# Optimization experiments

Measured on AMD Instinct MI355X. Metric: run time of the kernel, lower is better.

## Reference

```python
import jax, jax.numpy as jnp
import numpy as np

B, S, D_MODEL, HEADS = 2, 2048, 1024, 16
K_D = D_MODEL // HEADS


def setup_inputs() -> dict:
    key = jax.random.key(0)
    ks = jax.random.split(key, 5)
    x = jax.random.normal(ks[0], (B, S, D_MODEL), dtype=jnp.float32)
    # causal mask, 1 = keep, 0 = masked (GPT-2 style)
    mask = jnp.tril(jnp.ones((S, S), dtype=jnp.int32))[None, None, :, :]
    sc = 0.02
    w_attn = jax.random.normal(ks[1], (D_MODEL, 3 * D_MODEL), dtype=jnp.float32) * sc
    b_attn = jax.random.normal(ks[2], (3 * D_MODEL,), dtype=jnp.float32) * sc
    w_proj = jax.random.normal(ks[3], (D_MODEL, D_MODEL), dtype=jnp.float32) * sc
    b_proj = jax.random.normal(ks[4], (D_MODEL,), dtype=jnp.float32) * sc
    return {"x": x, "mask": mask, "w_attn": w_attn, "b_attn": b_attn,
            "w_proj": w_proj, "b_proj": b_proj}


def reference(x, mask, w_attn, b_attn, w_proj, b_proj):
    b, s, _ = x.shape
    qkv = x @ w_attn + b_attn                      # [B,S,3*d_model]
    # NOTE: source assigns value, query, key = split(...) in that order
    v, q, k = jnp.split(qkv, 3, axis=-1)
    def heads(t):  # [B,S,d_model] -> [B,H,S,k_d]
        return t.reshape(b, s, HEADS, K_D).transpose(0, 2, 1, 3)
    v, q, k = heads(v), heads(q), heads(k)
    present = jnp.stack((k, v))                    # [2,B,H,S,k_d]
    scores = jnp.einsum('bhqd,bhkd->bhqk', q, k) / jnp.sqrt(jnp.float32(K_D))
    scores = jnp.where(mask == 0, -jnp.inf, scores)
    attn = jax.nn.softmax(scores, axis=-1)         # [B,H,S,S]
    out = jnp.einsum('bhqk,bhkd->bhqd', attn, v)   # [B,H,S,k_d]
    out = out.transpose(0, 2, 1, 3).reshape(b, s, D_MODEL)
    out = out @ w_proj + b_proj
    return out, present
```

## Files before the change

### kernel.cpp

```cpp
#include <hip/hip_runtime.h>
#include <math.h>

constexpr int BB = 2;
constexpr int SS = 2048;
constexpr int DM = 1024;
constexpr int NH = 16;
constexpr int KD = 64;
constexpr int OUT_ELEMS  = BB*SS*DM;
constexpr int PRES_HALF  = BB*NH*SS*KD;
#define NEGSENT (-1e30f)

typedef __attribute__((ext_vector_type(8))) short short8;
typedef __attribute__((ext_vector_type(4))) short short4v;
typedef __attribute__((ext_vector_type(4))) float f32x4;

__device__ __forceinline__ float us2f(unsigned short u) {
  union { unsigned int ui; float f; } c; c.ui = ((unsigned int)u) << 16; return c.f;
}
__device__ __forceinline__ short f2s(float f) {
  union { float f; unsigned int u; } c; c.f = f;
  return (short)((c.u + 0x7FFFu + ((c.u >> 16) & 1u)) >> 16);
}

#define GLOAD_LDS16(g, l) \
  __builtin_amdgcn_global_load_lds((const __attribute__((address_space(1))) void*)(g), \
                                   (__attribute__((address_space(3))) void*)(l), 16, 0, 0)

__global__ __launch_bounds__(256)
void cast_x_k(const float* __restrict__ x, short* __restrict__ xb) {
  const size_t i = ((size_t)blockIdx.x * 256 + threadIdx.x) * 4;
  const float4 v = *(const float4*)(x + i);
  short4v s; s.x = f2s(v.x); s.y = f2s(v.y); s.z = f2s(v.z); s.w = f2s(v.w);
  *(short4v*)(xb + i) = s;
}

__global__ __launch_bounds__(256)
void transpose_k(const float* __restrict__ w, int N, short* __restrict__ wt) {
  __shared__ float tl[32][33];
  const int tx = threadIdx.x & 31, ty = threadIdx.x >> 5;
  const int n0 = blockIdx.x * 32, k0 = blockIdx.y * 32;
  #pragma unroll
  for (int i = 0; i < 4; ++i) {
    const int kk = ty + i * 8;
    tl[kk][tx] = w[(size_t)(k0 + kk) * N + n0 + tx];
  }
  __syncthreads();
  #pragma unroll
  for (int i = 0; i < 4; ++i) {
    const int nn = ty + i * 8;
    wt[(size_t)(n0 + nn) * 1024 + k0 + tx] = f2s(tl[tx][nn]);
  }
}

__device__ __forceinline__ void mfma_tile_loop(
    const short* __restrict__ A, const short* __restrict__ Bt,
    int m0, int n0, short* Asm, short* Bsm, f32x4 (*acc)[4]) {
  const int tid = threadIdx.x;
  const int lane = tid & 63;
  const int w = tid >> 6;
  const int wm = (w >> 1) * 64, wn = (w & 1) * 64;
  const int ln15 = lane & 15, quad = lane >> 4;
  for (int k0 = 0; k0 < 1024; k0 += 32) {
    #pragma unroll
    for (int j = 0; j < 2; ++j) {
      const int e = j * 256 + tid;
      const int r = e >> 2, cq = e & 3;
      GLOAD_LDS16(A  + (size_t)(m0 + r) * 1024 + k0 + cq * 8, Asm + e * 8);
      GLOAD_LDS16(Bt + (size_t)(n0 + r) * 1024 + k0 + cq * 8, Bsm + e * 8);
    }
    __syncthreads();
    short8 af[4], bf[4];
    #pragma unroll
    for (int t = 0; t < 4; ++t)
      af[t] = *(const short8*)(Asm + (wm + t * 16 + ln15) * 32 + quad * 8);
    #pragma unroll
    for (int t = 0; t < 4; ++t)
      bf[t] = *(const short8*)(Bsm + (wn + t * 16 + ln15) * 32 + quad * 8);
    #pragma unroll
    for (int tm = 0; tm < 4; ++tm)
      #pragma unroll
      for (int tn = 0; tn < 4; ++tn)
        acc[tm][tn] = __builtin_amdgcn_mfma_f32_16x16x32_bf16(
            af[tm], bf[tn], acc[tm][tn], 0, 0, 0);
    __syncthreads();
  }
}

__global__ __launch_bounds__(256)
void qkv_mfma_k(const short* __restrict__ A, const short* __restrict__ Bt,
                const float* __restrict__ bias, short* __restrict__ qbf,
                float* __restrict__ outf, short* __restrict__ kbf,
                short* __restrict__ vbft) {
  __shared__ short Asm[128 * 32];
  __shared__ short Bsm[128 * 32];
  const int n0 = blockIdx.x * 128, m0 = blockIdx.y * 128;
  f32x4 acc[4][4] = {};
  mfma_tile_loop(A, Bt, m0, n0, Asm, Bsm, acc);
  const int lane = threadIdx.x & 63;
  const int w = threadIdx.x >> 6;
  const int wm = (w >> 1) * 64, wn = (w & 1) * 64;
  const int col = lane & 15, row4 = (lane >> 4) * 4;
  #pragma unroll
  for (int tm = 0; tm < 4; ++tm) {
    #pragma unroll
    for (int tn = 0; tn < 4; ++tn) {
      const int n = n0 + wn + tn * 16 + col;
      #pragma unroll
      for (int r = 0; r < 4; ++r) {
        const int m = m0 + wm + tm * 16 + row4 + r;
        const float val = acc[tm][tn][r] + bias[n];
        const int bb = m >> 11, s = m & 2047;
        const int c = n & 1023, h = c >> 6, d = c & 63;
        const size_t idx = ((size_t)(bb * NH + h) * SS + s) * KD + d;
        if (n < DM) {
          outf[(size_t)OUT_ELEMS + (size_t)PRES_HALF + idx] = val;
          if (kbf) vbft[((size_t)(bb * NH + h) * KD + d) * SS + s] = f2s(val);
        } else if (n < 2 * DM) {
          qbf[idx] = f2s(val);
        } else {
          outf[(size_t)OUT_ELEMS + idx] = val;
          if (kbf) kbf[idx] = f2s(val);
        }
      }
    }
  }
}

__global__ __launch_bounds__(256)
void proj_mfma_k(const short* __restrict__ A, const short* __restrict__ Bt,
                 const float* __restrict__ bias, float* __restrict__ outf) {
  __shared__ short Asm[128 * 32];
  __shared__ short Bsm[128 * 32];
  const int n0 = blockIdx.x * 128, m0 = blockIdx.y * 128;
  f32x4 acc[4][4] = {};
  mfma_tile_loop(A, Bt, m0, n0, Asm, Bsm, acc);
  const int lane = threadIdx.x & 63;
  const int w = threadIdx.x >> 6;
  const int wm = (w >> 1) * 64, wn = (w & 1) * 64;
  const int col = lane & 15, row4 = (lane >> 4) * 4;
  #pragma unroll
  for (int tm = 0; tm < 4; ++tm) {
    #pragma unroll
    for (int tn = 0; tn < 4; ++tn) {
      const int n = n0 + wn + tn * 16 + col;
      const float b = bias[n];
      #pragma unroll
      for (int r = 0; r < 4; ++r) {
        const int m = m0 + wm + tm * 16 + row4 + r;
        outf[(size_t)m * DM + n] = acc[tm][tn][r] + b;
      }
    }
  }
}

__device__ __forceinline__ void stage_kv4(const short* __restrict__ Kg,
                                          const short* __restrict__ Vg,
                                          int kb, short* Ksb, short* Vtb,
                                          int tid) {
  #pragma unroll
  for (int rd = 0; rd < 2; ++rd) {
    const int i = rd * 256 + tid;
    const int row = i >> 3, grp = i & 7;
    const int sw = (grp ^ (row & 7)) << 3;
    GLOAD_LDS16(Kg + (size_t)(kb + row) * KD + sw, Ksb + i * 8);
    GLOAD_LDS16(Vg + (size_t)row * SS + kb + sw, Vtb + i * 8);
  }
}

__global__ __launch_bounds__(256)
void attn_mfma5_k(const short* __restrict__ qbf, const short* __restrict__ kbf,
                  const short* __restrict__ vbft, short* __restrict__ obf) {
  __shared__ short Ks[2][64 * 64];
  __shared__ short Vt[2][64 * 64];
  __shared__ short Ps[4][16 * 64];
  const int bid = blockIdx.x;
  const int xcd = bid & 7, g = bid >> 3;
  const int rr  = g & 31, rnd = g >> 5;
  const int bh  = (xcd << 2) | rnd;
  const int qb  = (rnd & 1) ? rr : 31 - rr;
  const int q0  = qb * 64;
  const int tid = threadIdx.x;
  const int w   = tid >> 6;
  const int lane = tid & 63;
  const int ln15 = lane & 15, quad = lane >> 4;
  const int rswz = (ln15 & 7) << 3;
  const float SC2 = 0.125f * 1.44269504f;

  short8 aq[2];
  {
    const short* qp = qbf + ((size_t)bh * SS + q0 + w * 16) * KD;
    aq[0] = *(const short8*)(qp + (size_t)ln15 * KD + quad * 8);
    aq[1] = *(const short8*)(qp + (size_t)ln15 * KD + 32 + quad * 8);
  }
  f32x4 O[4] = {};
  float mreg[4], lreg[4];
  #pragma unroll
  for (int r = 0; r < 4; ++r) { mreg[r] = NEGSENT; lreg[r] = 0.f; }

  const short* Kg = kbf  + (size_t)bh * SS * KD;
  const short* Vg = vbft + (size_t)bh * KD * SS;
  short* Pw = Ps[w];
  const int nch = qb + 1;

  stage_kv4(Kg, Vg, 0, Ks[0], Vt[0], tid);
  __syncthreads();

  for (int ch = 0; ch < nch; ++ch) {
    const int cur = ch & 1;
    if (ch + 1 < nch)
      stage_kv4(Kg, Vg, (ch + 1) * 64, Ks[cur ^ 1], Vt[cur ^ 1], tid);
    const short* Kc = Ks[cur];
    const short* Vc = Vt[cur];

    f32x4 S[4] = {};
    #pragma unroll
    for (int kt = 0; kt < 2; ++kt) {
      short8 bk[4];
      #pragma unroll
      for (int tn = 0; tn < 4; ++tn)
        bk[tn] = *(const short8*)(Kc + (tn * 16 + ln15) * 64 + ((kt * 32 + quad * 8) ^ rswz));
      #pragma unroll
      for (int tn = 0; tn < 4; ++tn)
        S[tn] = __builtin_amdgcn_mfma_f32_16x16x32_bf16(aq[kt], bk[tn], S[tn], 0, 0, 0);
    }

    if (ch == qb) {
      const int rowl = w * 16 + quad * 4;
      #pragma unroll
      for (int tn = 0; tn < 4; ++tn) {
        const int colk = tn * 16 + ln15;
        #pragma unroll
        for (int r = 0; r < 4; ++r)
          if (colk > rowl + r) S[tn][r] = NEGSENT;
      }
    }

    float alph[4];
    #pragma unroll
    for (int r = 0; r < 4; ++r) {
      float mx = fmaxf(fmaxf(S[0][r], S[1][r]), fmaxf(S[2][r], S[3][r]));
      mx = fmaxf(mx, __shfl_xor(mx, 1, 64));
      mx = fmaxf(mx, __shfl_xor(mx, 2, 64));
      mx = fmaxf(mx, __shfl_xor(mx, 4, 64));
      mx = fmaxf(mx, __shfl_xor(mx, 8, 64));
      const float mn = fmaxf(mreg[r], mx);
      alph[r] = exp2f((mreg[r] - mn) * SC2);
      mreg[r] = mn;
    }
    #pragma unroll
    for (int r = 0; r < 4; ++r) {
      const float mn = mreg[r], al = alph[r];
      const int prow = quad * 4 + r;
      const int rs = (prow & 7) << 3;
      float p0 = exp2f((S[0][r] - mn) * SC2);
      float p1 = exp2f((S[1][r] - mn) * SC2);
      float p2 = exp2f((S[2][r] - mn) * SC2);
      float p3 = exp2f((S[3][r] - mn) * SC2);
      lreg[r] = lreg[r] * al + ((p0 + p1) + (p2 + p3));
      Pw[prow * 64 + ((0 * 16 + ln15) ^ rs)] = f2s(p0);
      Pw[prow * 64 + ((1 * 16 + ln15) ^ rs)] = f2s(p1);
      Pw[prow * 64 + ((2 * 16 + ln15) ^ rs)] = f2s(p2);
      Pw[prow * 64 + ((3 * 16 + ln15) ^ rs)] = f2s(p3);
      O[0][r] *= al; O[1][r] *= al; O[2][r] *= al; O[3][r] *= al;
    }
    asm volatile("s_waitcnt lgkmcnt(0)" ::: "memory");
    __builtin_amdgcn_sched_barrier(0);

    #pragma unroll
    for (int kt = 0; kt < 2; ++kt) {
      short8 ap = *(const short8*)(Pw + ln15 * 64 + ((kt * 32 + quad * 8) ^ rswz));
      short8 bv[4];
      #pragma unroll
      for (int tn = 0; tn < 4; ++tn)
        bv[tn] = *(const short8*)(Vc + (tn * 16 + ln15) * 64 + ((kt * 32 + quad * 8) ^ rswz));
      #pragma unroll
      for (int tn = 0; tn < 4; ++tn)
        O[tn] = __builtin_amdgcn_mfma_f32_16x16x32_bf16(ap, bv[tn], O[tn], 0, 0, 0);
    }
    __syncthreads();
  }

  #pragma unroll
  for (int r = 0; r < 4; ++r) {
    float l = lreg[r];
    l += __shfl_xor(l, 1, 64);
    l += __shfl_xor(l, 2, 64);
    l += __shfl_xor(l, 4, 64);
    l += __shfl_xor(l, 8, 64);
    lreg[r] = 1.f / fmaxf(l, 1e-30f);
  }
  const int bb = bh >> 4, h = bh & 15;
  short* ob = obf + ((size_t)bb * SS + q0 + w * 16) * DM + h * KD;
  #pragma unroll
  for (int tn = 0; tn < 4; ++tn)
    #pragma unroll
    for (int r = 0; r < 4; ++r)
      ob[(size_t)(quad * 4 + r) * DM + tn * 16 + ln15] = f2s(O[tn][r] * lreg[r]);
}

__global__ __launch_bounds__(256)
void attn_k(const short* __restrict__ qbf, const float* __restrict__ pres,
            short* __restrict__ obf) {
  __shared__ float Ksf[32][64];
  __shared__ float Vsf[32][64];
  const int bh = blockIdx.x;
  const int q0 = ((int)gridDim.y - 1 - (int)blockIdx.y) * 64;
  const int t  = threadIdx.x;
  const int part = t & 3;
  const int row  = t >> 2;
  const int qr   = q0 + row;
  const int dbase = part * 16;
  const size_t qoff = ((size_t)bh * SS + qr) * KD + dbase;
  float q[16], o[16];
  #pragma unroll
  for (int i = 0; i < 16; ++i) q[i] = us2f((unsigned short)qbf[qoff + i]);
  #pragma unroll
  for (int i = 0; i < 16; ++i) o[i] = 0.f;
  float m = NEGSENT, l = 0.f;
  const float* Kb = pres + (size_t)bh * SS * KD;
  const float* Vb = pres + (size_t)PRES_HALF + (size_t)bh * SS * KD;
  const int nch = (q0 + 64) / 32;
  for (int ch = 0; ch < nch; ++ch) {
    const int kbase = ch * 32;
    __syncthreads();
    {
      const float4* ksrc = (const float4*)(Kb + (size_t)kbase * KD);
      const float4* vsrc = (const float4*)(Vb + (size_t)kbase * KD);
      float4* kdst = (float4*)&Ksf[0][0];
      float4* vdst = (float4*)&Vsf[0][0];
      #pragma unroll
      for (int i = 0; i < 2; ++i) {
        kdst[t + i * 256] = ksrc[t + i * 256];
        vdst[t + i * 256] = vsrc[t + i * 256];
      }
    }
    __syncthreads();
    float sc[32];
    #pragma unroll
    for (int kk = 0; kk < 32; ++kk) {
      float s = 0.f;
      #pragma unroll
      for (int i = 0; i < 16; ++i) s = fmaf(q[i], Ksf[kk][dbase + i], s);
      s += __shfl_xor(s, 1, 64);
      s += __shfl_xor(s, 2, 64);
      sc[kk] = (kbase + kk <= qr) ? s * 0.125f : NEGSENT;
    }
    float mc = sc[0];
    #pragma unroll
    for (int kk = 1; kk < 32; ++kk) mc = fmaxf(mc, sc[kk]);
    const float mn = fmaxf(m, mc);
    const float alpha = __expf(m - mn);
    l *= alpha;
    #pragma unroll
    for (int i = 0; i < 16; ++i) o[i] *= alpha;
    #pragma unroll
    for (int kk = 0; kk < 32; ++kk) {
      const float p = __expf(sc[kk] - mn);
      l += p;
      #pragma unroll
      for (int i = 0; i < 16; ++i) o[i] = fmaf(p, Vsf[kk][dbase + i], o[i]);
    }
    m = mn;
  }
  const float inv = 1.f / fmaxf(l, 1e-30f);
  const int bb = bh >> 4, h = bh & 15;
  const size_t ooff = ((size_t)(bb * SS + qr)) * DM + h * KD + dbase;
  #pragma unroll
  for (int i = 0; i < 16; ++i) obf[ooff + i] = f2s(o[i] * inv);
}

extern "C" void kernel_launch(void* const* d_in, const int* in_sizes, int n_in,
                              void* d_out, int out_size, void* d_ws, size_t ws_size,
                              hipStream_t stream) {
  const float* x      = (const float*)d_in[0];
  const float* w_attn = (const float*)d_in[2];
  const float* b_attn = (const float*)d_in[3];
  const float* w_proj = (const float*)d_in[4];
  const float* b_proj = (const float*)d_in[5];
  float* outf = (float*)d_out;

  constexpr size_t MB = 1024 * 1024;
  if (ws_size >= 24 * MB) {
    short* ws0   = (short*)d_ws;
    short* x_bf  = ws0;
    short* o_bf  = ws0;
    short* wat_t = ws0 + (size_t)4 * 1024 * 1024;
    short* wpt_t = ws0 + (size_t)7 * 1024 * 1024;
    short* q_bf  = ws0 + (size_t)8 * 1024 * 1024;
    short* k_bf  = (short*)d_out;
    short* v_bft = k_bf + (size_t)PRES_HALF;

    cast_x_k<<<4096, 256, 0, stream>>>(x, x_bf);
    transpose_k<<<dim3(96, 32), 256, 0, stream>>>(w_attn, 3 * DM, wat_t);
    transpose_k<<<dim3(32, 32), 256, 0, stream>>>(w_proj, DM, wpt_t);

    qkv_mfma_k<<<dim3(24, 32), 256, 0, stream>>>(x_bf, wat_t, b_attn, q_bf, outf,
                                                 k_bf, v_bft);

    attn_mfma5_k<<<dim3(BB * NH * (SS / 64)), 256, 0, stream>>>(q_bf, k_bf, v_bft, o_bf);

    proj_mfma_k<<<dim3(8, 32), 256, 0, stream>>>(o_bf, wpt_t, b_proj, outf);
  } else {
    short* x_bf;
    short* q_bf;
    short* wat_t;
    short* wpt_t;
    short* o_bf;
    if (ws_size >= 16 * MB) {
      short* ws = (short*)d_ws;
      x_bf  = (short*)d_out;
      q_bf  = x_bf + OUT_ELEMS;
      wat_t = ws;
      wpt_t = wat_t + 3 * DM * DM;
      o_bf  = wat_t + 4 * DM * DM;
    } else {
      x_bf  = (short*)d_out;
      q_bf  = x_bf + OUT_ELEMS;
      wat_t = (short*)d_in[1];
      wpt_t = wat_t + 3 * DM * DM;
      o_bf  = wat_t + 4 * DM * DM;
    }
    cast_x_k<<<4096, 256, 0, stream>>>(x, x_bf);
    transpose_k<<<dim3(96, 32), 256, 0, stream>>>(w_attn, 3 * DM, wat_t);
    transpose_k<<<dim3(32, 32), 256, 0, stream>>>(w_proj, DM, wpt_t);
    qkv_mfma_k<<<dim3(24, 32), 256, 0, stream>>>(x_bf, wat_t, b_attn, q_bf, outf,
                                                 nullptr, nullptr);
    attn_k<<<dim3(BB * NH, SS / 64), 256, 0, stream>>>(q_bf, outf + OUT_ELEMS, o_bf);
    proj_mfma_k<<<dim3(8, 32), 256, 0, stream>>>(o_bf, wpt_t, b_proj, outf);
  }
}
```

Baseline: 236.7 us.

## Double GEMM K-tile depth and add lazy softmax rescaling in attention

The shared MFMA GEMM loop now stages a 64-wide K slice per iteration instead of 32. That halves the number of barrier pairs and global-to-LDS rounds but doubles the LDS footprint. The attention kernel now rescales the running max, sum and O accumulators only when some row's new chunk max exceeds the stored max by more than a threshold (checked wave-wide), so the per-chunk alpha exp and rescale multiplies are usually skipped. The exponent is folded into an fma. The threshold bounds growth of the unnormalized probabilities, but any row whose max rises by less than the threshold keeps a stale max, so its exponents can exceed 1. This slightly changes numerics and the bf16 P rounding.

```diff
diff --git a/kernel.cpp b/kernel.cpp
--- a/kernel.cpp
+++ b/kernel.cpp
@@ -60,28 +60,31 @@
   const int w = tid >> 6;
   const int wm = (w >> 1) * 64, wn = (w & 1) * 64;
   const int ln15 = lane & 15, quad = lane >> 4;
-  for (int k0 = 0; k0 < 1024; k0 += 32) {
-    #pragma unroll
-    for (int j = 0; j < 2; ++j) {
+  for (int k0 = 0; k0 < 1024; k0 += 64) {
+    #pragma unroll
+    for (int j = 0; j < 4; ++j) {
       const int e = j * 256 + tid;
-      const int r = e >> 2, cq = e & 3;
+      const int r = e >> 3, cq = e & 7;
       GLOAD_LDS16(A  + (size_t)(m0 + r) * 1024 + k0 + cq * 8, Asm + e * 8);
       GLOAD_LDS16(Bt + (size_t)(n0 + r) * 1024 + k0 + cq * 8, Bsm + e * 8);
     }
     __syncthreads();
-    short8 af[4], bf[4];
-    #pragma unroll
-    for (int t = 0; t < 4; ++t)
-      af[t] = *(const short8*)(Asm + (wm + t * 16 + ln15) * 32 + quad * 8);
-    #pragma unroll
-    for (int t = 0; t < 4; ++t)
-      bf[t] = *(const short8*)(Bsm + (wn + t * 16 + ln15) * 32 + quad * 8);
-    #pragma unroll
-    for (int tm = 0; tm < 4; ++tm)
-      #pragma unroll
-      for (int tn = 0; tn < 4; ++tn)
-        acc[tm][tn] = __builtin_amdgcn_mfma_f32_16x16x32_bf16(
-            af[tm], bf[tn], acc[tm][tn], 0, 0, 0);
+    #pragma unroll
+    for (int kk = 0; kk < 2; ++kk) {
+      short8 af[4], bf[4];
+      #pragma unroll
+      for (int t = 0; t < 4; ++t)
+        af[t] = *(const short8*)(Asm + (wm + t * 16 + ln15) * 64 + kk * 32 + quad * 8);
+      #pragma unroll
+      for (int t = 0; t < 4; ++t)
+        bf[t] = *(const short8*)(Bsm + (wn + t * 16 + ln15) * 64 + kk * 32 + quad * 8);
+      #pragma unroll
+      for (int tm = 0; tm < 4; ++tm)
+        #pragma unroll
+        for (int tn = 0; tn < 4; ++tn)
+          acc[tm][tn] = __builtin_amdgcn_mfma_f32_16x16x32_bf16(
+              af[tm], bf[tn], acc[tm][tn], 0, 0, 0);
+    }
     __syncthreads();
   }
 }
@@ -91,8 +94,8 @@
                 const float* __restrict__ bias, short* __restrict__ qbf,
                 float* __restrict__ outf, short* __restrict__ kbf,
                 short* __restrict__ vbft) {
-  __shared__ short Asm[128 * 32];
-  __shared__ short Bsm[128 * 32];
+  __shared__ short Asm[128 * 64];
+  __shared__ short Bsm[128 * 64];
   const int n0 = blockIdx.x * 128, m0 = blockIdx.y * 128;
   f32x4 acc[4][4] = {};
   mfma_tile_loop(A, Bt, m0, n0, Asm, Bsm, acc);
@@ -129,8 +132,8 @@
 __global__ __launch_bounds__(256)
 void proj_mfma_k(const short* __restrict__ A, const short* __restrict__ Bt,
                  const float* __restrict__ bias, float* __restrict__ outf) {
-  __shared__ short Asm[128 * 32];
-  __shared__ short Bsm[128 * 32];
+  __shared__ short Asm[128 * 64];
+  __shared__ short Bsm[128 * 64];
   const int n0 = blockIdx.x * 128, m0 = blockIdx.y * 128;
   f32x4 acc[4][4] = {};
   mfma_tile_loop(A, Bt, m0, n0, Asm, Bsm, acc);
@@ -168,7 +171,7 @@
 }
 
 __global__ __launch_bounds__(256)
-void attn_mfma5_k(const short* __restrict__ qbf, const short* __restrict__ kbf,
+void attn_mfma6_k(const short* __restrict__ qbf, const short* __restrict__ kbf,
                   const short* __restrict__ vbft, short* __restrict__ obf) {
   __shared__ short Ks[2][64 * 64];
   __shared__ short Vt[2][64 * 64];
@@ -185,6 +188,7 @@
   const int ln15 = lane & 15, quad = lane >> 4;
   const int rswz = (ln15 & 7) << 3;
   const float SC2 = 0.125f * 1.44269504f;
+  const float THR = 8.0f;
 
   short8 aq[2];
   {
@@ -235,33 +239,45 @@
       }
     }
 
-    float alph[4];
+    float pmax[4];
     #pragma unroll
     for (int r = 0; r < 4; ++r) {
-      float mx = fmaxf(fmaxf(S[0][r], S[1][r]), fmaxf(S[2][r], S[3][r]));
+      float mx = fmaxf(fmaxf(fmaxf(S[0][r], S[1][r]), S[2][r]), S[3][r]);
       mx = fmaxf(mx, __shfl_xor(mx, 1, 64));
       mx = fmaxf(mx, __shfl_xor(mx, 2, 64));
       mx = fmaxf(mx, __shfl_xor(mx, 4, 64));
       mx = fmaxf(mx, __shfl_xor(mx, 8, 64));
-      const float mn = fmaxf(mreg[r], mx);
-      alph[r] = exp2f((mreg[r] - mn) * SC2);
-      mreg[r] = mn;
-    }
+      pmax[r] = mx;
+    }
+
+    bool okl = true;
+    #pragma unroll
+    for (int r = 0; r < 4; ++r) okl = okl && (pmax[r] - mreg[r] <= THR);
+    if (!__all((int)okl)) {
+      #pragma unroll
+      for (int r = 0; r < 4; ++r) {
+        const float mn = fmaxf(mreg[r], pmax[r]);
+        const float al = exp2f((mreg[r] - mn) * SC2);
+        mreg[r] = mn;
+        lreg[r] *= al;
+        O[0][r] *= al; O[1][r] *= al; O[2][r] *= al; O[3][r] *= al;
+      }
+    }
+
     #pragma unroll
     for (int r = 0; r < 4; ++r) {
-      const float mn = mreg[r], al = alph[r];
+      const float mnsc = mreg[r] * SC2;
       const int prow = quad * 4 + r;
       const int rs = (prow & 7) << 3;
-      float p0 = exp2f((S[0][r] - mn) * SC2);
-      float p1 = exp2f((S[1][r] - mn) * SC2);
-      float p2 = exp2f((S[2][r] - mn) * SC2);
-      float p3 = exp2f((S[3][r] - mn) * SC2);
-      lreg[r] = lreg[r] * al + ((p0 + p1) + (p2 + p3));
+      float p0 = exp2f(fmaf(S[0][r], SC2, -mnsc));
+      float p1 = exp2f(fmaf(S[1][r], SC2, -mnsc));
+      float p2 = exp2f(fmaf(S[2][r], SC2, -mnsc));
+      float p3 = exp2f(fmaf(S[3][r], SC2, -mnsc));
+      lreg[r] += (p0 + p1) + (p2 + p3);
       Pw[prow * 64 + ((0 * 16 + ln15) ^ rs)] = f2s(p0);
       Pw[prow * 64 + ((1 * 16 + ln15) ^ rs)] = f2s(p1);
       Pw[prow * 64 + ((2 * 16 + ln15) ^ rs)] = f2s(p2);
       Pw[prow * 64 + ((3 * 16 + ln15) ^ rs)] = f2s(p3);
-      O[0][r] *= al; O[1][r] *= al; O[2][r] *= al; O[3][r] *= al;
     }
     asm volatile("s_waitcnt lgkmcnt(0)" ::: "memory");
     __builtin_amdgcn_sched_barrier(0);
@@ -397,7 +413,7 @@
     qkv_mfma_k<<<dim3(24, 32), 256, 0, stream>>>(x_bf, wat_t, b_attn, q_bf, outf,
                                                  k_bf, v_bft);
 
-    attn_mfma5_k<<<dim3(BB * NH * (SS / 64)), 256, 0, stream>>>(q_bf, k_bf, v_bft, o_bf);
+    attn_mfma6_k<<<dim3(BB * NH * (SS / 64)), 256, 0, stream>>>(q_bf, k_bf, v_bft, o_bf);
 
     proj_mfma_k<<<dim3(8, 32), 256, 0, stream>>>(o_bf, wpt_t, b_proj, outf);
   } else {
```

Result: slower. 261.9 us (+10.7%).
